# Performance work log

Measured on AMD Instinct MI355X. Metric: run time of the kernel, lower is better.

Reference implementation:

```python
import jax, jax.numpy as jnp
import numpy as np

LAMBDA_E_SUM = 10.0
LAMBDA_HIT = 20.0
LAMBDA_CHAMFER = 1e-3
LAMBDA_HIT_ENTROPY = 0.1
EPS = 1e-6
BIG = 1e18


def setup_inputs() -> dict:
    key = jax.random.key(0)
    ks = jax.random.split(key, 7)
    B, Np, Ng, L = 32, 2048, 2048, 256
    pred_feat = jax.random.normal(ks[0], (B, 4, Np), dtype=jnp.float32)
    # hit-probability channel must be in (0,1) (sigmoid head in the real model)
    pred_hit = jax.random.uniform(ks[1], (B, 1, Np), dtype=jnp.float32,
                                  minval=1e-4, maxval=1.0 - 1e-4)
    preds = jnp.concatenate([pred_feat, pred_hit], axis=1)          # [B,5,Np]
    target = jax.random.normal(ks[2], (B, 4, Ng), dtype=jnp.float32)  # [B,4,Ng]
    target_mask = (jax.random.uniform(ks[3], (B, Ng)) < 0.9).astype(jnp.float32)
    mu = jax.random.normal(ks[4], (B, L), dtype=jnp.float32)
    logvar = 0.5 * jax.random.normal(ks[5], (B, L), dtype=jnp.float32)
    e_init = jax.random.uniform(ks[6], (B,), dtype=jnp.float32,
                                minval=10.0, maxval=100.0)
    kl_weight = jnp.float32(1e-3)
    return {"preds": preds, "target": target, "target_mask": target_mask,
            "mu": mu, "logvar": logvar, "e_init": e_init,
            "kl_weight": kl_weight}


def reference(preds, target, target_mask, mu, logvar, e_init, kl_weight):
    B = preds.shape[0]
    preds_t = jnp.swapaxes(preds, 1, 2)    # [B, Np, 5]
    target_t = jnp.swapaxes(target, 1, 2)  # [B, Ng, 4]
    pred_xyz = preds_t[..., :3]            # [B, Np, 3]
    pred_E = preds_t[..., 3]               # [B, Np]
    pred_hit = preds_t[..., 4]             # [B, Np]
    target_xyz = target_t[..., :3]         # [B, Ng, 3]
    target_E = target_t[..., 3]            # [B, Ng]

    # squared pairwise distances [B, Np, Ng]
    pn = jnp.sum(pred_xyz * pred_xyz, axis=-1)      # [B, Np]
    tn = jnp.sum(target_xyz * target_xyz, axis=-1)  # [B, Ng]
    dist_sq = jnp.maximum(
        pn[:, :, None] + tn[:, None, :]
        - 2.0 * jnp.einsum('bnd,bmd->bnm', pred_xyz, target_xyz), 0.0)

    inf_mask = target_mask[:, None, :] == 0.0       # [B, 1->Np, Ng]
    dist_sq_masked = jnp.where(inf_mask, BIG, dist_sq)
    min_dist_pred = jnp.min(dist_sq_masked, axis=2)     # [B, Np]
    idx_pred = jnp.argmin(dist_sq_masked, axis=2)       # [B, Np]
    min_dist_target = jnp.min(dist_sq, axis=1)          # [B, Ng]

    mask_sum = jnp.sum(target_mask)
    loss_chamfer_target = jnp.sum(min_dist_target * target_mask) / mask_sum
    loss_chamfer_pred = jnp.mean(min_dist_pred)
    loss_chamfer = loss_chamfer_target + loss_chamfer_pred

    matched_target_E = jnp.take_along_axis(target_E, idx_pred, axis=1)  # [B, Np]
    loss_local_E = jnp.mean(jnp.abs(pred_E - matched_target_E))

    n_hits_pred = jnp.sum(pred_hit, axis=1)                 # [B]
    n_hits_target = jnp.sum(target_mask, axis=1)            # [B]
    loss_hit_count = jnp.mean((n_hits_pred - n_hits_target) ** 2)

    loss_hit_entropy = -jnp.mean(pred_hit * jnp.log(pred_hit + EPS)
                                 + (1.0 - pred_hit) * jnp.log(1.0 - pred_hit + EPS))

    total_pred_E = jnp.sum(pred_E * pred_hit, axis=1)       # [B]
    loss_global_E_sum = jnp.mean((total_pred_E - e_init) ** 2)

    loss_kld = -0.5 * jnp.sum(1.0 + logvar - mu * mu - jnp.exp(logvar)) / B

    loss_chamf = loss_chamfer * LAMBDA_CHAMFER
    losskld = kl_weight * loss_kld
    loss_global_e = LAMBDA_E_SUM * loss_global_E_sum
    loss_hit = LAMBDA_HIT * loss_hit_count
    loss_hit_entr = LAMBDA_HIT_ENTROPY * loss_hit_entropy

    total_loss = (loss_chamf + loss_local_E + losskld
                  + loss_global_e + loss_hit + loss_hit_entr)
    components = jnp.stack([loss_chamf, loss_local_E, loss_global_e,
                            loss_hit, losskld])
    return total_loss, components
```

## Files before the change

### kernel.cpp

```cpp
#include <hip/hip_runtime.h>

#define BB 32
#define NP 2048
#define NG 2048
#define LDIM 256
#define EPSF 1e-6f
#define BIGF 1e18f
#define FLTMAX 3.4e38f
#define MT 128

#define ACC_FLOATS 104
#define PRED_OFF 4096
#define TGT_OFF (4096 + NP * BB * 8)


__global__ __launch_bounds__(256) void k_pred(const float* __restrict__ preds,
                                              const float* __restrict__ target,
                                              const float* __restrict__ mask,
                                              unsigned long long* __restrict__ pmin) {
  __shared__ float4 t4[MT];
  const int bx = blockIdx.x;
  const int b = bx >> 5;
  const int nch = (bx >> 4) & 1;
  const int mp = bx & 15;
  const int tid = threadIdx.x;
  const float* tb = target + b * 4 * NG;
  const int mbase = mp * MT;
  if (tid < MT) {
    int m = mbase + tid;
    float tx = tb[m], ty = tb[NG + m], tz = tb[2 * NG + m];
    float tn = fmaf(tx, tx, fmaf(ty, ty, tz * tz));
    float w = tn + (mask[b * NG + m] == 0.0f ? BIGF : 0.0f);
    t4[tid] = make_float4(-2.0f * tx, -2.0f * ty, -2.0f * tz, w);
  }
  __syncthreads();

  const int n0 = nch * 1024 + tid;
  const float* pb = preds + b * 5 * NP;
  const float px0 = pb[n0], py0 = pb[NP + n0], pz0 = pb[2 * NP + n0];
  const float px1 = pb[n0 + 256], py1 = pb[NP + n0 + 256], pz1 = pb[2 * NP + n0 + 256];
  const float px2 = pb[n0 + 512], py2 = pb[NP + n0 + 512], pz2 = pb[2 * NP + n0 + 512];
  const float px3 = pb[n0 + 768], py3 = pb[NP + n0 + 768], pz3 = pb[2 * NP + n0 + 768];

  float b0a = FLTMAX, b0b = FLTMAX, b1a = FLTMAX, b1b = FLTMAX;
  float b2a = FLTMAX, b2b = FLTMAX, b3a = FLTMAX, b3b = FLTMAX;
  int i0a = 0, i0b = 0, i1a = 0, i1b = 0, i2a = 0, i2b = 0, i3a = 0, i3b = 0;
#pragma unroll 4
  for (int m = 0; m < MT; m += 2) {
    float4 t = t4[m];
    float4 u = t4[m + 1];
    float s0a = fmaf(px0, t.x, fmaf(py0, t.y, fmaf(pz0, t.z, t.w)));
    float s1a = fmaf(px1, t.x, fmaf(py1, t.y, fmaf(pz1, t.z, t.w)));
    float s2a = fmaf(px2, t.x, fmaf(py2, t.y, fmaf(pz2, t.z, t.w)));
    float s3a = fmaf(px3, t.x, fmaf(py3, t.y, fmaf(pz3, t.z, t.w)));
    float s0b = fmaf(px0, u.x, fmaf(py0, u.y, fmaf(pz0, u.z, u.w)));
    float s1b = fmaf(px1, u.x, fmaf(py1, u.y, fmaf(pz1, u.z, u.w)));
    float s2b = fmaf(px2, u.x, fmaf(py2, u.y, fmaf(pz2, u.z, u.w)));
    float s3b = fmaf(px3, u.x, fmaf(py3, u.y, fmaf(pz3, u.z, u.w)));
    if (s0a < b0a) { b0a = s0a; i0a = m; }
    if (s1a < b1a) { b1a = s1a; i1a = m; }
    if (s2a < b2a) { b2a = s2a; i2a = m; }
    if (s3a < b3a) { b3a = s3a; i3a = m; }
    if (s0b < b0b) { b0b = s0b; i0b = m + 1; }
    if (s1b < b1b) { b1b = s1b; i1b = m + 1; }
    if (s2b < b2b) { b2b = s2b; i2b = m + 1; }
    if (s3b < b3b) { b3b = s3b; i3b = m + 1; }
  }

  float pn0 = fmaf(px0, px0, fmaf(py0, py0, pz0 * pz0));
  float pn1 = fmaf(px1, px1, fmaf(py1, py1, pz1 * pz1));
  float pn2 = fmaf(px2, px2, fmaf(py2, py2, pz2 * pz2));
  float pn3 = fmaf(px3, px3, fmaf(py3, py3, pz3 * pz3));
  float bv; int bi;
  unsigned long long* base = &pmin[b * NP];

  if (b0b < b0a || (b0b == b0a && i0b < i0a)) { bv = b0b; bi = i0b; } else { bv = b0a; bi = i0a; }
  atomicMin(&base[n0], ((unsigned long long)__float_as_uint(fmaxf(bv + pn0, 0.0f)) << 32) | (unsigned)(mbase + bi));
  if (b1b < b1a || (b1b == b1a && i1b < i1a)) { bv = b1b; bi = i1b; } else { bv = b1a; bi = i1a; }
  atomicMin(&base[n0 + 256], ((unsigned long long)__float_as_uint(fmaxf(bv + pn1, 0.0f)) << 32) | (unsigned)(mbase + bi));
  if (b2b < b2a || (b2b == b2a && i2b < i2a)) { bv = b2b; bi = i2b; } else { bv = b2a; bi = i2a; }
  atomicMin(&base[n0 + 512], ((unsigned long long)__float_as_uint(fmaxf(bv + pn2, 0.0f)) << 32) | (unsigned)(mbase + bi));
  if (b3b < b3a || (b3b == b3a && i3b < i3a)) { bv = b3b; bi = i3b; } else { bv = b3a; bi = i3a; }
  atomicMin(&base[n0 + 768], ((unsigned long long)__float_as_uint(fmaxf(bv + pn3, 0.0f)) << 32) | (unsigned)(mbase + bi));
}

__global__ __launch_bounds__(256) void k_tgt(const float* __restrict__ preds,
                                             const float* __restrict__ target,
                                             unsigned* __restrict__ tmin) {
  __shared__ float4 p4[MT];
  const int bx = blockIdx.x;
  const int b = bx >> 5;
  const int mch = (bx >> 4) & 1;
  const int np_ = bx & 15;
  const int tid = threadIdx.x;
  const float* pb = preds + b * 5 * NP;
  if (tid < MT) {
    int n = np_ * MT + tid;
    float px = pb[n], py = pb[NP + n], pz = pb[2 * NP + n];
    float pn2 = fmaf(px, px, fmaf(py, py, pz * pz));
    p4[tid] = make_float4(-2.0f * px, -2.0f * py, -2.0f * pz, pn2);
  }
  __syncthreads();

  const int m0 = mch * 1024 + tid;
  const float* tb = target + b * 4 * NG;
  const float tx0 = tb[m0], ty0 = tb[NG + m0], tz0 = tb[2 * NG + m0];
  const float tx1 = tb[m0 + 256], ty1 = tb[NG + m0 + 256], tz1 = tb[2 * NG + m0 + 256];
  const float tx2 = tb[m0 + 512], ty2 = tb[NG + m0 + 512], tz2 = tb[2 * NG + m0 + 512];
  const float tx3 = tb[m0 + 768], ty3 = tb[NG + m0 + 768], tz3 = tb[2 * NG + m0 + 768];

  float b0a = FLTMAX, b0b = FLTMAX, b1a = FLTMAX, b1b = FLTMAX;
  float b2a = FLTMAX, b2b = FLTMAX, b3a = FLTMAX, b3b = FLTMAX;
#pragma unroll 4
  for (int n = 0; n < MT; n += 2) {
    float4 p = p4[n];
    float4 q = p4[n + 1];
    b0a = fminf(b0a, fmaf(tx0, p.x, fmaf(ty0, p.y, fmaf(tz0, p.z, p.w))));
    b1a = fminf(b1a, fmaf(tx1, p.x, fmaf(ty1, p.y, fmaf(tz1, p.z, p.w))));
    b2a = fminf(b2a, fmaf(tx2, p.x, fmaf(ty2, p.y, fmaf(tz2, p.z, p.w))));
    b3a = fminf(b3a, fmaf(tx3, p.x, fmaf(ty3, p.y, fmaf(tz3, p.z, p.w))));
    b0b = fminf(b0b, fmaf(tx0, q.x, fmaf(ty0, q.y, fmaf(tz0, q.z, q.w))));
    b1b = fminf(b1b, fmaf(tx1, q.x, fmaf(ty1, q.y, fmaf(tz1, q.z, q.w))));
    b2b = fminf(b2b, fmaf(tx2, q.x, fmaf(ty2, q.y, fmaf(tz2, q.z, q.w))));
    b3b = fminf(b3b, fmaf(tx3, q.x, fmaf(ty3, q.y, fmaf(tz3, q.z, q.w))));
  }
  float tn0 = fmaf(tx0, tx0, fmaf(ty0, ty0, tz0 * tz0));
  float tn1 = fmaf(tx1, tx1, fmaf(ty1, ty1, tz1 * tz1));
  float tn2 = fmaf(tx2, tx2, fmaf(ty2, ty2, tz2 * tz2));
  float tn3 = fmaf(tx3, tx3, fmaf(ty3, ty3, tz3 * tz3));
  unsigned* base = &tmin[b * NG];
  atomicMin(&base[m0], __float_as_uint(fmaxf(fminf(b0a, b0b) + tn0, 0.0f)));
  atomicMin(&base[m0 + 256], __float_as_uint(fmaxf(fminf(b1a, b1b) + tn1, 0.0f)));
  atomicMin(&base[m0 + 512], __float_as_uint(fmaxf(fminf(b2a, b2b) + tn2, 0.0f)));
  atomicMin(&base[m0 + 768], __float_as_uint(fmaxf(fminf(b3a, b3b) + tn3, 0.0f)));
}

__global__ __launch_bounds__(256) void k_fin(const unsigned long long* __restrict__ pmin,
                                             const unsigned* __restrict__ tmin,
                                             const float* __restrict__ preds,
                                             const float* __restrict__ target,
                                             const float* __restrict__ mask,
                                             const float* __restrict__ mu,
                                             const float* __restrict__ logvar,
                                             float* __restrict__ acc) {
  __shared__ float red[4][8];
  const int bx = blockIdx.x;
  const int tid = threadIdx.x;
  const int wave = tid >> 6, lane = tid & 63;
  float q0 = 0.0f, q1 = 0.0f, q2 = 0.0f, q3 = 0.0f, q4 = 0.0f;
  int nq, a0, a1, a2, a3 = 0, a4 = 0;

  if (bx < 128) {
    const int b = bx >> 2;
    const float* pb = preds + b * 5 * NP;
    const float* te = target + b * 4 * NG + 3 * NG;
#pragma unroll
    for (int e = 0; e < 2; e++) {
      int i = bx * 512 + e * 256 + tid;
      int n = i & 2047;
      unsigned long long pk = pmin[i];
      float best = __uint_as_float((unsigned)(pk >> 32));
      int idx = (int)(pk & 0xffffffffu);
      float mE = te[idx];
      float pE = pb[3 * NP + n];
      float ph = pb[4 * NP + n];
      q0 += best;
      q1 += fabsf(pE - mE);
      q2 += ph * logf(ph + EPSF) + (1.0f - ph) * logf(1.0f - ph + EPSF);
      q3 += ph;
      q4 += pE * ph;
    }
    nq = 5; a0 = 0; a1 = 1; a2 = 2; a3 = 8 + b; a4 = 40 + b;
  } else if (bx < 256) {
    const int bb = bx - 128;
    const int b = bb >> 2;
#pragma unroll
    for (int e = 0; e < 2; e++) {
      int i = bb * 512 + e * 256 + tid;
      float d = __uint_as_float(tmin[i]);
      float msk = mask[i];
      q0 += d * msk;
      q1 += msk;
      q2 += msk;
    }
    nq = 3; a0 = 3; a1 = 4; a2 = 72 + b;
  } else {
    const int bb = bx - 256;
#pragma unroll
    for (int e = 0; e < 4; e++) {
      int i = bb * 1024 + e * 256 + tid;
      float m = mu[i], lv = logvar[i];
      q0 += 1.0f + lv - m * m - expf(lv);
    }
    nq = 1; a0 = 5; a1 = 0; a2 = 0;
  }

  float qs[5] = {q0, q1, q2, q3, q4};
  int ai[5] = {a0, a1, a2, a3, a4};
  for (int k = 0; k < nq; k++) {
    float v = qs[k];
    v += __shfl_down(v, 32);
    v += __shfl_down(v, 16);
    v += __shfl_down(v, 8);
    v += __shfl_down(v, 4);
    v += __shfl_down(v, 2);
    v += __shfl_down(v, 1);
    if (lane == 0) red[wave][k] = v;
  }
  __syncthreads();
  if (tid < nq) {
    float s = red[0][tid] + red[1][tid] + red[2][tid] + red[3][tid];
    atomicAdd(&acc[ai[tid]], s);
  }
}

__global__ __launch_bounds__(64) void k_final(const float* __restrict__ acc,
                                              const float* __restrict__ e_init,
                                              const float* __restrict__ kl_weight,
                                              float* __restrict__ out) {
  int t = threadIdx.x;
  float hitsq = 0.0f, esq = 0.0f;
  if (t < BB) {
    float dh = acc[8 + t] - acc[72 + t];
    hitsq = dh * dh;
    float de = acc[40 + t] - e_init[t];
    esq = de * de;
  }
  for (int o = 32; o > 0; o >>= 1) {
    hitsq += __shfl_down(hitsq, o);
    esq += __shfl_down(esq, o);
  }
  if (t == 0) {
    const float invBN = 1.0f / (float)(BB * NP);
    float chamfer_pred = acc[0] * invBN;
    float localE = acc[1] * invBN;
    float ent = -acc[2] * invBN;
    float chamfer_tgt = acc[3] / acc[4];
    float kld = -0.5f * acc[5] / (float)BB;
    float hit = hitsq / (float)BB;
    float ge = esq / (float)BB;

    float loss_chamf = (chamfer_tgt + chamfer_pred) * 0.001f;
    float losskld = kl_weight[0] * kld;
    float loss_ge = 10.0f * ge;
    float loss_hit = 20.0f * hit;
    float loss_ent = 0.1f * ent;

    float total = loss_chamf + localE + losskld + loss_ge + loss_hit + loss_ent;
    out[0] = total;
    out[1] = loss_chamf;
    out[2] = localE;
    out[3] = loss_ge;
    out[4] = loss_hit;
    out[5] = losskld;
  }
}

extern "C" void kernel_launch(void* const* d_in, const int* in_sizes, int n_in,
                              void* d_out, int out_size, void* d_ws, size_t ws_size,
                              hipStream_t stream) {
  const float* preds = (const float*)d_in[0];
  const float* target = (const float*)d_in[1];
  const float* mask = (const float*)d_in[2];
  const float* mu = (const float*)d_in[3];
  const float* logvar = (const float*)d_in[4];
  const float* e_init = (const float*)d_in[5];
  const float* kl_weight = (const float*)d_in[6];
  float* acc = (float*)d_ws;
  unsigned long long* pmin = (unsigned long long*)((char*)d_ws + PRED_OFF);
  unsigned* tmin = (unsigned*)((char*)d_ws + TGT_OFF);
  float* out = (float*)d_out;

  hipMemsetAsync(acc, 0, ACC_FLOATS * sizeof(float), stream);
  hipMemsetAsync((char*)d_ws + PRED_OFF, 0xFF,
                 (size_t)BB * NP * 8 + (size_t)BB * NG * 4, stream);

  k_pred<<<1024, 256, 0, stream>>>(preds, target, mask, pmin);
  k_tgt<<<1024, 256, 0, stream>>>(preds, target, tmin);
  k_fin<<<264, 256, 0, stream>>>(pmin, tmin, preds, target, mask, mu, logvar, acc);
  k_final<<<1, 64, 0, stream>>>(acc, e_init, kl_weight, out);
}
```

Before: 109.5 us.

## Replace atomic min reductions with per-tile partial buffers and fuse pairwise kernels

```diff
diff --git a/kernel.cpp b/kernel.cpp
--- a/kernel.cpp
+++ b/kernel.cpp
@@ -3,152 +3,109 @@
 #define BB 32
 #define NP 2048
 #define NG 2048
-#define LDIM 256
 #define EPSF 1e-6f
 #define BIGF 1e18f
 #define FLTMAX 3.4e38f
 #define MT 128
-
-#define ACC_FLOATS 104
-#define PRED_OFF 4096
-#define TGT_OFF (4096 + NP * BB * 8)
-
-
-__global__ __launch_bounds__(256) void k_pred(const float* __restrict__ preds,
-                                              const float* __restrict__ target,
-                                              const float* __restrict__ mask,
-                                              unsigned long long* __restrict__ pmin) {
-  __shared__ float4 t4[MT];
+#define MP 16
+
+#define FPART_OFF 0
+#define PPART_OFF 65536
+#define TPART_OFF (65536 + BB * MP * NP * 8)
+
+__global__ __launch_bounds__(256, 8) void k_pair(const float* __restrict__ preds,
+                                                 const float* __restrict__ target,
+                                                 const float* __restrict__ mask,
+                                                 unsigned long long* __restrict__ ppart,
+                                                 float* __restrict__ tpart) {
+  __shared__ float4 s4[MT];
   const int bx = blockIdx.x;
-  const int b = bx >> 5;
-  const int nch = (bx >> 4) & 1;
-  const int mp = bx & 15;
   const int tid = threadIdx.x;
-  const float* tb = target + b * 4 * NG;
-  const int mbase = mp * MT;
-  if (tid < MT) {
-    int m = mbase + tid;
-    float tx = tb[m], ty = tb[NG + m], tz = tb[2 * NG + m];
-    float tn = fmaf(tx, tx, fmaf(ty, ty, tz * tz));
-    float w = tn + (mask[b * NG + m] == 0.0f ? BIGF : 0.0f);
-    t4[tid] = make_float4(-2.0f * tx, -2.0f * ty, -2.0f * tz, w);
-  }
-  __syncthreads();
-
-  const int n0 = nch * 1024 + tid;
-  const float* pb = preds + b * 5 * NP;
-  const float px0 = pb[n0], py0 = pb[NP + n0], pz0 = pb[2 * NP + n0];
-  const float px1 = pb[n0 + 256], py1 = pb[NP + n0 + 256], pz1 = pb[2 * NP + n0 + 256];
-  const float px2 = pb[n0 + 512], py2 = pb[NP + n0 + 512], pz2 = pb[2 * NP + n0 + 512];
-  const float px3 = pb[n0 + 768], py3 = pb[NP + n0 + 768], pz3 = pb[2 * NP + n0 + 768];
-
-  float b0a = FLTMAX, b0b = FLTMAX, b1a = FLTMAX, b1b = FLTMAX;
-  float b2a = FLTMAX, b2b = FLTMAX, b3a = FLTMAX, b3b = FLTMAX;
-  int i0a = 0, i0b = 0, i1a = 0, i1b = 0, i2a = 0, i2b = 0, i3a = 0, i3b = 0;
-#pragma unroll 4
-  for (int m = 0; m < MT; m += 2) {
-    float4 t = t4[m];
-    float4 u = t4[m + 1];
-    float s0a = fmaf(px0, t.x, fmaf(py0, t.y, fmaf(pz0, t.z, t.w)));
-    float s1a = fmaf(px1, t.x, fmaf(py1, t.y, fmaf(pz1, t.z, t.w)));
-    float s2a = fmaf(px2, t.x, fmaf(py2, t.y, fmaf(pz2, t.z, t.w)));
-    float s3a = fmaf(px3, t.x, fmaf(py3, t.y, fmaf(pz3, t.z, t.w)));
-    float s0b = fmaf(px0, u.x, fmaf(py0, u.y, fmaf(pz0, u.z, u.w)));
-    float s1b = fmaf(px1, u.x, fmaf(py1, u.y, fmaf(pz1, u.z, u.w)));
-    float s2b = fmaf(px2, u.x, fmaf(py2, u.y, fmaf(pz2, u.z, u.w)));
-    float s3b = fmaf(px3, u.x, fmaf(py3, u.y, fmaf(pz3, u.z, u.w)));
-    if (s0a < b0a) { b0a = s0a; i0a = m; }
-    if (s1a < b1a) { b1a = s1a; i1a = m; }
-    if (s2a < b2a) { b2a = s2a; i2a = m; }
-    if (s3a < b3a) { b3a = s3a; i3a = m; }
-    if (s0b < b0b) { b0b = s0b; i0b = m + 1; }
-    if (s1b < b1b) { b1b = s1b; i1b = m + 1; }
-    if (s2b < b2b) { b2b = s2b; i2b = m + 1; }
-    if (s3b < b3b) { b3b = s3b; i3b = m + 1; }
-  }
-
-  float pn0 = fmaf(px0, px0, fmaf(py0, py0, pz0 * pz0));
-  float pn1 = fmaf(px1, px1, fmaf(py1, py1, pz1 * pz1));
-  float pn2 = fmaf(px2, px2, fmaf(py2, py2, pz2 * pz2));
-  float pn3 = fmaf(px3, px3, fmaf(py3, py3, pz3 * pz3));
-  float bv; int bi;
-  unsigned long long* base = &pmin[b * NP];
-
-  if (b0b < b0a || (b0b == b0a && i0b < i0a)) { bv = b0b; bi = i0b; } else { bv = b0a; bi = i0a; }
-  atomicMin(&base[n0], ((unsigned long long)__float_as_uint(fmaxf(bv + pn0, 0.0f)) << 32) | (unsigned)(mbase + bi));
-  if (b1b < b1a || (b1b == b1a && i1b < i1a)) { bv = b1b; bi = i1b; } else { bv = b1a; bi = i1a; }
-  atomicMin(&base[n0 + 256], ((unsigned long long)__float_as_uint(fmaxf(bv + pn1, 0.0f)) << 32) | (unsigned)(mbase + bi));
-  if (b2b < b2a || (b2b == b2a && i2b < i2a)) { bv = b2b; bi = i2b; } else { bv = b2a; bi = i2a; }
-  atomicMin(&base[n0 + 512], ((unsigned long long)__float_as_uint(fmaxf(bv + pn2, 0.0f)) << 32) | (unsigned)(mbase + bi));
-  if (b3b < b3a || (b3b == b3a && i3b < i3a)) { bv = b3b; bi = i3b; } else { bv = b3a; bi = i3a; }
-  atomicMin(&base[n0 + 768], ((unsigned long long)__float_as_uint(fmaxf(bv + pn3, 0.0f)) << 32) | (unsigned)(mbase + bi));
-}
-
-__global__ __launch_bounds__(256) void k_tgt(const float* __restrict__ preds,
-                                             const float* __restrict__ target,
-                                             unsigned* __restrict__ tmin) {
-  __shared__ float4 p4[MT];
-  const int bx = blockIdx.x;
-  const int b = bx >> 5;
-  const int mch = (bx >> 4) & 1;
-  const int np_ = bx & 15;
-  const int tid = threadIdx.x;
-  const float* pb = preds + b * 5 * NP;
-  if (tid < MT) {
-    int n = np_ * MT + tid;
-    float px = pb[n], py = pb[NP + n], pz = pb[2 * NP + n];
-    float pn2 = fmaf(px, px, fmaf(py, py, pz * pz));
-    p4[tid] = make_float4(-2.0f * px, -2.0f * py, -2.0f * pz, pn2);
-  }
-  __syncthreads();
-
-  const int m0 = mch * 1024 + tid;
-  const float* tb = target + b * 4 * NG;
-  const float tx0 = tb[m0], ty0 = tb[NG + m0], tz0 = tb[2 * NG + m0];
-  const float tx1 = tb[m0 + 256], ty1 = tb[NG + m0 + 256], tz1 = tb[2 * NG + m0 + 256];
-  const float tx2 = tb[m0 + 512], ty2 = tb[NG + m0 + 512], tz2 = tb[2 * NG + m0 + 512];
-  const float tx3 = tb[m0 + 768], ty3 = tb[NG + m0 + 768], tz3 = tb[2 * NG + m0 + 768];
-
-  float b0a = FLTMAX, b0b = FLTMAX, b1a = FLTMAX, b1b = FLTMAX;
-  float b2a = FLTMAX, b2b = FLTMAX, b3a = FLTMAX, b3b = FLTMAX;
-#pragma unroll 4
-  for (int n = 0; n < MT; n += 2) {
-    float4 p = p4[n];
-    float4 q = p4[n + 1];
-    b0a = fminf(b0a, fmaf(tx0, p.x, fmaf(ty0, p.y, fmaf(tz0, p.z, p.w))));
-    b1a = fminf(b1a, fmaf(tx1, p.x, fmaf(ty1, p.y, fmaf(tz1, p.z, p.w))));
-    b2a = fminf(b2a, fmaf(tx2, p.x, fmaf(ty2, p.y, fmaf(tz2, p.z, p.w))));
-    b3a = fminf(b3a, fmaf(tx3, p.x, fmaf(ty3, p.y, fmaf(tz3, p.z, p.w))));
-    b0b = fminf(b0b, fmaf(tx0, q.x, fmaf(ty0, q.y, fmaf(tz0, q.z, q.w))));
-    b1b = fminf(b1b, fmaf(tx1, q.x, fmaf(ty1, q.y, fmaf(tz1, q.z, q.w))));
-    b2b = fminf(b2b, fmaf(tx2, q.x, fmaf(ty2, q.y, fmaf(tz2, q.z, q.w))));
-    b3b = fminf(b3b, fmaf(tx3, q.x, fmaf(ty3, q.y, fmaf(tz3, q.z, q.w))));
-  }
-  float tn0 = fmaf(tx0, tx0, fmaf(ty0, ty0, tz0 * tz0));
-  float tn1 = fmaf(tx1, tx1, fmaf(ty1, ty1, tz1 * tz1));
-  float tn2 = fmaf(tx2, tx2, fmaf(ty2, ty2, tz2 * tz2));
-  float tn3 = fmaf(tx3, tx3, fmaf(ty3, ty3, tz3 * tz3));
-  unsigned* base = &tmin[b * NG];
-  atomicMin(&base[m0], __float_as_uint(fmaxf(fminf(b0a, b0b) + tn0, 0.0f)));
-  atomicMin(&base[m0 + 256], __float_as_uint(fmaxf(fminf(b1a, b1b) + tn1, 0.0f)));
-  atomicMin(&base[m0 + 512], __float_as_uint(fmaxf(fminf(b2a, b2b) + tn2, 0.0f)));
-  atomicMin(&base[m0 + 768], __float_as_uint(fmaxf(fminf(b3a, b3b) + tn3, 0.0f)));
-}
-
-__global__ __launch_bounds__(256) void k_fin(const unsigned long long* __restrict__ pmin,
-                                             const unsigned* __restrict__ tmin,
+
+  if (bx < 2048) {
+    const int b = bx >> 6;
+    const int nch = (bx >> 4) & 3;
+    const int mp = bx & 15;
+    const float* tb = target + b * 4 * NG;
+    const int mbase = mp * MT;
+    if (tid < MT) {
+      int m = mbase + tid;
+      float tx = tb[m], ty = tb[NG + m], tz = tb[2 * NG + m];
+      float tn = fmaf(tx, tx, fmaf(ty, ty, tz * tz));
+      float w = tn + (mask[b * NG + m] == 0.0f ? BIGF : 0.0f);
+      s4[tid] = make_float4(-2.0f * tx, -2.0f * ty, -2.0f * tz, w);
+    }
+    __syncthreads();
+
+    const int n0 = nch * 512 + tid;
+    const float* pb = preds + b * 5 * NP;
+    const float px0 = pb[n0], py0 = pb[NP + n0], pz0 = pb[2 * NP + n0];
+    const float px1 = pb[n0 + 256], py1 = pb[NP + n0 + 256], pz1 = pb[2 * NP + n0 + 256];
+
+    float b0 = FLTMAX, b1 = FLTMAX;
+    int i0 = 0, i1 = 0;
+#pragma unroll 2
+    for (int m = 0; m < MT; m++) {
+      float4 t = s4[m];
+      float s0 = fmaf(px0, t.x, fmaf(py0, t.y, fmaf(pz0, t.z, t.w)));
+      float s1 = fmaf(px1, t.x, fmaf(py1, t.y, fmaf(pz1, t.z, t.w)));
+      if (s0 < b0) { b0 = s0; i0 = m; }
+      if (s1 < b1) { b1 = s1; i1 = m; }
+    }
+    float pn0 = fmaf(px0, px0, fmaf(py0, py0, pz0 * pz0));
+    float pn1 = fmaf(px1, px1, fmaf(py1, py1, pz1 * pz1));
+    float d0 = fmaxf(b0 + pn0, 0.0f);
+    float d1 = fmaxf(b1 + pn1, 0.0f);
+    unsigned long long* row = &ppart[(b * MP + mp) * NP];
+    row[n0] = ((unsigned long long)__float_as_uint(d0) << 32) | (unsigned)(mbase + i0);
+    row[n0 + 256] = ((unsigned long long)__float_as_uint(d1) << 32) | (unsigned)(mbase + i1);
+  } else {
+    const int bb = bx - 2048;
+    const int b = bb >> 6;
+    const int mch = (bb >> 4) & 3;
+    const int np_ = bb & 15;
+    const float* pb = preds + b * 5 * NP;
+    if (tid < MT) {
+      int n = np_ * MT + tid;
+      float px = pb[n], py = pb[NP + n], pz = pb[2 * NP + n];
+      float pn2 = fmaf(px, px, fmaf(py, py, pz * pz));
+      s4[tid] = make_float4(-2.0f * px, -2.0f * py, -2.0f * pz, pn2);
+    }
+    __syncthreads();
+
+    const int m0 = mch * 512 + tid;
+    const float* tb = target + b * 4 * NG;
+    const float tx0 = tb[m0], ty0 = tb[NG + m0], tz0 = tb[2 * NG + m0];
+    const float tx1 = tb[m0 + 256], ty1 = tb[NG + m0 + 256], tz1 = tb[2 * NG + m0 + 256];
+
+    float c0 = FLTMAX, c1 = FLTMAX;
+#pragma unroll 2
+    for (int n = 0; n < MT; n++) {
+      float4 p = s4[n];
+      c0 = fminf(c0, fmaf(tx0, p.x, fmaf(ty0, p.y, fmaf(tz0, p.z, p.w))));
+      c1 = fminf(c1, fmaf(tx1, p.x, fmaf(ty1, p.y, fmaf(tz1, p.z, p.w))));
+    }
+    float tn0 = fmaf(tx0, tx0, fmaf(ty0, ty0, tz0 * tz0));
+    float tn1 = fmaf(tx1, tx1, fmaf(ty1, ty1, tz1 * tz1));
+    float* row = &tpart[(b * MP + np_) * NG];
+    row[m0] = fmaxf(c0 + tn0, 0.0f);
+    row[m0 + 256] = fmaxf(c1 + tn1, 0.0f);
+  }
+}
+
+__global__ __launch_bounds__(256) void k_fin(const unsigned long long* __restrict__ ppart,
+                                             const float* __restrict__ tpart,
                                              const float* __restrict__ preds,
                                              const float* __restrict__ target,
                                              const float* __restrict__ mask,
                                              const float* __restrict__ mu,
                                              const float* __restrict__ logvar,
-                                             float* __restrict__ acc) {
+                                             float* __restrict__ fpart) {
   __shared__ float red[4][8];
   const int bx = blockIdx.x;
   const int tid = threadIdx.x;
   const int wave = tid >> 6, lane = tid & 63;
   float q0 = 0.0f, q1 = 0.0f, q2 = 0.0f, q3 = 0.0f, q4 = 0.0f;
-  int nq, a0, a1, a2, a3 = 0, a4 = 0;
 
   if (bx < 128) {
     const int b = bx >> 2;
@@ -158,32 +115,40 @@
     for (int e = 0; e < 2; e++) {
       int i = bx * 512 + e * 256 + tid;
       int n = i & 2047;
-      unsigned long long pk = pmin[i];
-      float best = __uint_as_float((unsigned)(pk >> 32));
-      int idx = (int)(pk & 0xffffffffu);
+      unsigned long long best = 0xFFFFFFFFFFFFFFFFull;
+      const unsigned long long* col = &ppart[b * MP * NP + n];
+#pragma unroll
+      for (int mp = 0; mp < MP; mp++) {
+        unsigned long long v = col[mp * NP];
+        best = v < best ? v : best;
+      }
+      float bd = __uint_as_float((unsigned)(best >> 32));
+      int idx = (int)(best & 0xffffffffu);
       float mE = te[idx];
       float pE = pb[3 * NP + n];
       float ph = pb[4 * NP + n];
-      q0 += best;
+      q0 += bd;
       q1 += fabsf(pE - mE);
       q2 += ph * logf(ph + EPSF) + (1.0f - ph) * logf(1.0f - ph + EPSF);
       q3 += ph;
       q4 += pE * ph;
     }
-    nq = 5; a0 = 0; a1 = 1; a2 = 2; a3 = 8 + b; a4 = 40 + b;
   } else if (bx < 256) {
     const int bb = bx - 128;
     const int b = bb >> 2;
 #pragma unroll
     for (int e = 0; e < 2; e++) {
       int i = bb * 512 + e * 256 + tid;
-      float d = __uint_as_float(tmin[i]);
+      int m = i & 2047;
+      float d = FLTMAX;
+      const float* col = &tpart[b * MP * NG + m];
+#pragma unroll
+      for (int np_ = 0; np_ < MP; np_++) d = fminf(d, col[np_ * NG]);
       float msk = mask[i];
       q0 += d * msk;
       q1 += msk;
       q2 += msk;
     }
-    nq = 3; a0 = 3; a1 = 4; a2 = 72 + b;
   } else {
     const int bb = bx - 256;
 #pragma unroll
@@ -192,12 +157,10 @@
       float m = mu[i], lv = logvar[i];
       q0 += 1.0f + lv - m * m - expf(lv);
     }
-    nq = 1; a0 = 5; a1 = 0; a2 = 0;
   }
 
   float qs[5] = {q0, q1, q2, q3, q4};
-  int ai[5] = {a0, a1, a2, a3, a4};
-  for (int k = 0; k < nq; k++) {
+  for (int k = 0; k < 5; k++) {
     float v = qs[k];
     v += __shfl_down(v, 32);
     v += __shfl_down(v, 16);
@@ -208,37 +171,59 @@
     if (lane == 0) red[wave][k] = v;
   }
   __syncthreads();
-  if (tid < nq) {
-    float s = red[0][tid] + red[1][tid] + red[2][tid] + red[3][tid];
-    atomicAdd(&acc[ai[tid]], s);
-  }
-}
-
-__global__ __launch_bounds__(64) void k_final(const float* __restrict__ acc,
-                                              const float* __restrict__ e_init,
-                                              const float* __restrict__ kl_weight,
-                                              float* __restrict__ out) {
-  int t = threadIdx.x;
-  float hitsq = 0.0f, esq = 0.0f;
+  if (tid < 5) fpart[bx * 8 + tid] = red[0][tid] + red[1][tid] + red[2][tid] + red[3][tid];
+}
+
+__global__ __launch_bounds__(256) void k_final(const float* __restrict__ fpart,
+                                               const float* __restrict__ e_init,
+                                               const float* __restrict__ kl_weight,
+                                               float* __restrict__ out) {
+  __shared__ float red[4][8];
+  const int t = threadIdx.x;
+  const int wave = t >> 6, lane = t & 63;
+  float g[8] = {0, 0, 0, 0, 0, 0, 0, 0};
+  if (t < 128) {
+    const float* r = &fpart[t * 8];
+    g[0] = r[0]; g[1] = r[1]; g[2] = r[2];
+    const float* r2 = &fpart[(128 + t) * 8];
+    g[3] = r2[0]; g[4] = r2[1];
+  }
+  if (t < 8) g[5] = fpart[(256 + t) * 8];
   if (t < BB) {
-    float dh = acc[8 + t] - acc[72 + t];
-    hitsq = dh * dh;
-    float de = acc[40 + t] - e_init[t];
-    esq = de * de;
-  }
-  for (int o = 32; o > 0; o >>= 1) {
-    hitsq += __shfl_down(hitsq, o);
-    esq += __shfl_down(esq, o);
-  }
+    float hit = 0.0f, eh = 0.0f, mk = 0.0f;
+#pragma unroll
+    for (int k = 0; k < 4; k++) {
+      hit += fpart[(4 * t + k) * 8 + 3];
+      eh += fpart[(4 * t + k) * 8 + 4];
+      mk += fpart[(128 + 4 * t + k) * 8 + 2];
+    }
+    float dh = hit - mk;
+    g[6] = dh * dh;
+    float de = eh - e_init[t];
+    g[7] = de * de;
+  }
+  for (int k = 0; k < 8; k++) {
+    float v = g[k];
+    v += __shfl_down(v, 32);
+    v += __shfl_down(v, 16);
+    v += __shfl_down(v, 8);
+    v += __shfl_down(v, 4);
+    v += __shfl_down(v, 2);
+    v += __shfl_down(v, 1);
+    if (lane == 0) red[wave][k] = v;
+  }
+  __syncthreads();
   if (t == 0) {
+    float s[8];
+    for (int k = 0; k < 8; k++) s[k] = red[0][k] + red[1][k] + red[2][k] + red[3][k];
     const float invBN = 1.0f / (float)(BB * NP);
-    float chamfer_pred = acc[0] * invBN;
-    float localE = acc[1] * invBN;
-    float ent = -acc[2] * invBN;
-    float chamfer_tgt = acc[3] / acc[4];
-    float kld = -0.5f * acc[5] / (float)BB;
-    float hit = hitsq / (float)BB;
-    float ge = esq / (float)BB;
+    float chamfer_pred = s[0] * invBN;
+    float localE = s[1] * invBN;
+    float ent = -s[2] * invBN;
+    float chamfer_tgt = s[3] / s[4];
+    float kld = -0.5f * s[5] / (float)BB;
+    float hit = s[6] / (float)BB;
+    float ge = s[7] / (float)BB;
 
     float loss_chamf = (chamfer_tgt + chamfer_pred) * 0.001f;
     float losskld = kl_weight[0] * kld;
@@ -266,17 +251,12 @@
   const float* logvar = (const float*)d_in[4];
   const float* e_init = (const float*)d_in[5];
   const float* kl_weight = (const float*)d_in[6];
-  float* acc = (float*)d_ws;
-  unsigned long long* pmin = (unsigned long long*)((char*)d_ws + PRED_OFF);
-  unsigned* tmin = (unsigned*)((char*)d_ws + TGT_OFF);
+  float* fpart = (float*)((char*)d_ws + FPART_OFF);
+  unsigned long long* ppart = (unsigned long long*)((char*)d_ws + PPART_OFF);
+  float* tpart = (float*)((char*)d_ws + TPART_OFF);
   float* out = (float*)d_out;
 
-  hipMemsetAsync(acc, 0, ACC_FLOATS * sizeof(float), stream);
-  hipMemsetAsync((char*)d_ws + PRED_OFF, 0xFF,
-                 (size_t)BB * NP * 8 + (size_t)BB * NG * 4, stream);
-
-  k_pred<<<1024, 256, 0, stream>>>(preds, target, mask, pmin);
-  k_tgt<<<1024, 256, 0, stream>>>(preds, target, tmin);
-  k_fin<<<264, 256, 0, stream>>>(pmin, tmin, preds, target, mask, mu, logvar, acc);
-  k_final<<<1, 64, 0, stream>>>(acc, e_init, kl_weight, out);
-}
+  k_pair<<<4096, 256, 0, stream>>>(preds, target, mask, ppart, tpart);
+  k_fin<<<264, 256, 0, stream>>>(ppart, tpart, preds, target, mask, mu, logvar, fpart);
+  k_final<<<1, 256, 0, stream>>>(fpart, e_init, kl_weight, out);
+}
```

New measurement: 106.8 us. 2.4% less time.
